# Performance work log

Hardware: AMD Instinct MI355X
Metric: run time of the kernel (lower is better)

The kernel has to match this reference:

```python
import jax, jax.numpy as jnp
import numpy as np
import math

N_HEAD = 16


def setup_inputs() -> dict:
    key = jax.random.key(0)
    ks = jax.random.split(key, 4)
    B, S, D = 4, 2048, 1024
    x = jax.random.normal(ks[0], (B, S, D), dtype=jnp.float32)
    c_attn_w = jax.random.normal(ks[1], (D, 3 * D), dtype=jnp.float32) * 0.02
    c_attn_b = jnp.zeros((3 * D,), dtype=jnp.float32)
    c_proj_w = jax.random.normal(ks[2], (D, D), dtype=jnp.float32) * 0.02
    c_proj_b = jnp.zeros((D,), dtype=jnp.float32)
    # causal mask: True where attention is disallowed (future positions)
    mask_self_attention = jnp.triu(jnp.ones((S, S), dtype=bool), k=1)[None, None]
    return {"x": x, "c_attn_w": c_attn_w, "c_attn_b": c_attn_b,
            "c_proj_w": c_proj_w, "c_proj_b": c_proj_b,
            "mask_self_attention": mask_self_attention}


def reference(x, c_attn_w, c_attn_b, c_proj_w, c_proj_b, mask_self_attention):
    B, S, D = x.shape
    H = N_HEAD
    hd = D // H
    qkv = x @ c_attn_w + c_attn_b                      # [B,S,3D]
    q, k, v = jnp.split(qkv, 3, axis=-1)
    # split heads -> [B,H,S,hd]
    q = q.reshape(B, S, H, hd).transpose(0, 2, 1, 3)
    k = k.reshape(B, S, H, hd).transpose(0, 2, 1, 3)
    v = v.reshape(B, S, H, hd).transpose(0, 2, 1, 3)
    w = jnp.einsum('bhqd,bhkd->bhqk', q, k) / math.sqrt(hd)  # scale=True
    w = jnp.where(mask_self_attention, jnp.float32(-10000.0), w)
    w = jax.nn.softmax(w, axis=-1)
    a = jnp.einsum('bhqk,bhkd->bhqd', w, v)            # [B,H,S,hd]
    a = a.transpose(0, 2, 1, 3).reshape(B, S, D)       # merge heads
    return a @ c_proj_w + c_proj_b
```

## Files before the change

kernel.cpp:

```cpp
#include <hip/hip_runtime.h>
#include <cstdint>
#include <cstddef>

#define S_LEN 2048
#define D_MODEL 1024
#define HD 64

typedef __attribute__((ext_vector_type(8))) __bf16 bf16x8;
typedef __attribute__((ext_vector_type(8))) unsigned short u16x8;
typedef __attribute__((ext_vector_type(4))) float f32x4;
typedef __attribute__((ext_vector_type(4))) unsigned short u16x4;

static __device__ __forceinline__ unsigned short f32_bf16(float f) {
    unsigned int u = __float_as_uint(f);
    u += 0x7fffu + ((u >> 16) & 1u);
    return (unsigned short)(u >> 16);
}

static __device__ __forceinline__ unsigned short f32_bf16_rn(float f) {
    return __builtin_bit_cast(unsigned short, (__bf16)f);
}

static __device__ __forceinline__ float fast_exp2(float x) {
#if __has_builtin(__builtin_amdgcn_exp2f)
    return __builtin_amdgcn_exp2f(x);
#else
    float r; asm("v_exp_f32 %0, %1" : "=v"(r) : "v"(x)); return r;
#endif
}

static __device__ __forceinline__ void gload_lds16(const void* g, void* l) {
    __builtin_amdgcn_global_load_lds(
        (const __attribute__((address_space(1))) unsigned int*)g,
        (__attribute__((address_space(3))) unsigned int*)l,
        16, 0, 0);
}

static __device__ __forceinline__ bf16x8 frag8(const unsigned short* p) {
    return __builtin_bit_cast(bf16x8, *(const u16x8*)p);
}

__global__ void prep_k(const float* __restrict__ x, unsigned short* __restrict__ xb,
                       const float* __restrict__ caw, unsigned short* __restrict__ wqt,
                       const float* __restrict__ cpw, unsigned short* __restrict__ wpt)
{
    __shared__ float tile[32][33];
    const int blk = blockIdx.x;
    const int tid = threadIdx.x;
    if (blk < 8192) {
        int i = blk * 256 + tid;
        f32x4 v = ((const f32x4*)x)[i];
        u16x4 o;
        o[0] = f32_bf16(v[0]); o[1] = f32_bf16(v[1]);
        o[2] = f32_bf16(v[2]); o[3] = f32_bf16(v[3]);
        ((u16x4*)xb)[i] = o;
        return;
    }
    const float* in; unsigned short* out; int R, C, bx, by;
    if (blk < 11264) {
        int t = blk - 8192; in = caw; out = wqt; R = 1024; C = 3072;
        bx = t % 96; by = t / 96;
    } else {
        int t = blk - 11264; in = cpw; out = wpt; R = 1024; C = 1024;
        bx = t & 31; by = t >> 5;
    }
    int tx = tid & 31, ty = tid >> 5;
    int x0 = bx * 32, y0 = by * 32;
#pragma unroll
    for (int p = 0; p < 32; p += 8)
        tile[ty + p][tx] = in[(size_t)(y0 + ty + p) * C + x0 + tx];
    __syncthreads();
#pragma unroll
    for (int p = 0; p < 32; p += 8)
        out[(size_t)(x0 + ty + p) * R + y0 + tx] = f32_bf16(tile[tx][ty + p]);
}

__device__ __forceinline__ void gemm128_mainloop(
    const unsigned short* __restrict__ A,
    const unsigned short* __restrict__ Bt,
    unsigned short* As, unsigned short* Bs,
    int m0, int n0, int Kdim, f32x4 acc[][4])
{
    const int tid = threadIdx.x;
    const int lane = tid & 63, wave = tid >> 6;
    const int wm = wave & 1, wn = wave >> 1;
    const int quad = lane >> 4, l15 = lane & 15;
    const int srow = wave * 8 + (lane >> 3);
    const int scol = ((lane & 7) ^ (lane >> 3)) * 8;
    const unsigned short* Ag = A + (size_t)(m0 + srow) * Kdim + scol;
    const unsigned short* Bg = Bt + (size_t)(n0 + srow) * Kdim + scol;
    unsigned short* Asw = As + (wave * 8) * 64 + lane * 8;
    unsigned short* Bsw = Bs + (wave * 8) * 64 + lane * 8;
    const int mkey = l15 & 7;

    for (int k0 = 0; k0 < Kdim; k0 += 64) {
        __syncthreads();
#pragma unroll
        for (int p = 0; p < 4; ++p)
            gload_lds16(Ag + (size_t)(p * 32) * Kdim + k0, Asw + (p * 32) * 64);
#pragma unroll
        for (int p = 0; p < 4; ++p)
            gload_lds16(Bg + (size_t)(p * 32) * Kdim + k0, Bsw + (p * 32) * 64);
        __syncthreads();
#pragma unroll
        for (int kh = 0; kh < 2; ++kh) {
            bf16x8 af[4], bfv[4];
#pragma unroll
            for (int i = 0; i < 4; ++i)
                af[i] = frag8(As + (wm * 64 + i * 16 + l15) * 64 +
                              ((((kh << 2) + quad) ^ mkey) << 3));
#pragma unroll
            for (int j = 0; j < 4; ++j)
                bfv[j] = frag8(Bs + (wn * 64 + j * 16 + l15) * 64 +
                               ((((kh << 2) + quad) ^ mkey) << 3));
#pragma unroll
            for (int i = 0; i < 4; ++i)
#pragma unroll
                for (int j = 0; j < 4; ++j)
                    acc[i][j] = __builtin_amdgcn_mfma_f32_16x16x32_bf16(
                        af[i], bfv[j], acc[i][j], 0, 0, 0);
        }
    }
}

__global__ __launch_bounds__(256, 2) void gemm_qkv_k(
    const unsigned short* __restrict__ xb,
    const unsigned short* __restrict__ wt,
    const float* __restrict__ bias,
    unsigned short* __restrict__ q,
    unsigned short* __restrict__ k2,
    unsigned short* __restrict__ vt)
{
    __shared__ unsigned short Sh[128 * 132];
    unsigned short* As = Sh;
    unsigned short* Bs = Sh + 128 * 64;
    const int lin = blockIdx.x + 24 * blockIdx.y;
    const int swz = (lin & 7) * 192 + (lin >> 3);
    const int n0 = (swz % 24) * 128, m0 = (swz / 24) * 128;
    f32x4 acc[4][4] = {};
    gemm128_mainloop(xb, wt, As, Bs, m0, n0, 1024, acc);

    const int tid = threadIdx.x;
    const int lane = tid & 63, wave = tid >> 6;
    const int wm = wave & 1, wn = wave >> 1;
    const int quad = lane >> 4, l15 = lane & 15;
    const bool isq = (n0 < 1024);
    const bool isv = (n0 >= 2048);
    const int cb = n0 & 1023;

    if (!isv) {
        unsigned short* outp = isq ? q : k2;
#pragma unroll
        for (int j = 0; j < 4; ++j) {
            int ct = cb + wn * 64 + j * 16 + l15;
            int h = ct >> 6, d = ct & 63;
            float bv = bias[n0 + wn * 64 + j * 16 + l15];
#pragma unroll
            for (int i = 0; i < 4; ++i)
#pragma unroll
                for (int r = 0; r < 4; ++r) {
                    int row = m0 + wm * 64 + i * 16 + quad * 4 + r;
                    int bb = row >> 11, s = row & 2047;
                    float val = acc[i][j][r] + bv;
                    if (isq) val *= 0.1803368801111244f;
                    outp[((size_t)(bb * 16 + h) * S_LEN + s) * HD + d] = f32_bf16(val);
                }
        }
    } else {
        __syncthreads();
#pragma unroll
        for (int j = 0; j < 4; ++j) {
            float bv = bias[n0 + wn * 64 + j * 16 + l15];
            int lc = wn * 64 + j * 16 + l15;
#pragma unroll
            for (int i = 0; i < 4; ++i)
#pragma unroll
                for (int r = 0; r < 4; ++r) {
                    int lr = wm * 64 + i * 16 + quad * 4 + r;
                    Sh[lr * 132 + lc] = f32_bf16(acc[i][j][r] + bv);
                }
        }
        __syncthreads();
        const int lc = (tid & 63) + (wave & 1) * 64;
        const int sh2 = wave >> 1;
        const int bb = m0 >> 11;
        const int s0 = (m0 & 2047) + sh2 * 64;
        const int bh = bb * 16 + (cb >> 6) + (lc >> 6);
        unsigned short* vp = vt + ((size_t)bh * HD + (lc & 63)) * S_LEN + s0;
#pragma unroll
        for (int k8 = 0; k8 < 8; ++k8) {
            u16x8 w;
#pragma unroll
            for (int e = 0; e < 8; ++e)
                w[e] = Sh[(sh2 * 64 + k8 * 8 + e) * 132 + lc];
            *(u16x8*)(vp + k8 * 8) = w;
        }
    }
}

__global__ __launch_bounds__(256, 2) void gemm_proj_k(
    const unsigned short* __restrict__ am,
    const unsigned short* __restrict__ wpt,
    const float* __restrict__ bias,
    float* __restrict__ out)
{
    __shared__ unsigned short As[128 * 64], Bs[128 * 64];
    const int lin = blockIdx.x + 8 * blockIdx.y;
    const int swz = (lin & 7) * 64 + (lin >> 3);
    const int n0 = (swz % 8) * 128, m0 = (swz / 8) * 128;
    f32x4 acc[4][4] = {};
    gemm128_mainloop(am, wpt, As, Bs, m0, n0, 1024, acc);

    const int lane = threadIdx.x & 63, wave = threadIdx.x >> 6;
    const int wm = wave & 1, wn = wave >> 1;
    const int quad = lane >> 4, l15 = lane & 15;
#pragma unroll
    for (int j = 0; j < 4; ++j) {
        int col = n0 + wn * 64 + j * 16 + l15;
        float bv = bias[col];
#pragma unroll
        for (int i = 0; i < 4; ++i)
#pragma unroll
            for (int r = 0; r < 4; ++r) {
                int row = m0 + wm * 64 + i * 16 + quad * 4 + r;
                out[(size_t)row * 1024 + col] = acc[i][j][r] + bv;
            }
    }
}

#define PSTR 72
__global__ __launch_bounds__(256, 3) void flash_attn_k(
    const unsigned short* __restrict__ Q,
    const unsigned short* __restrict__ K,
    const unsigned short* __restrict__ Vt,
    unsigned short* __restrict__ Am)
{
    __shared__ unsigned short Ps[4 * 32 * PSTR];
    __shared__ unsigned short Ks[2][64 * 64];
    __shared__ unsigned short Vs[2][64 * 64];

    const int bid = blockIdx.x;
    const int xcd = bid & 7;
    const int w = bid >> 3;
    const int qt = 15 - (w >> 3);
    const int bh = xcd * 8 + (w & 7);
    const int b = bh >> 4, h = bh & 15;
    const int tid = threadIdx.x;
    const int lane = tid & 63, wave = tid >> 6;
    const int quad = lane >> 4, l15 = lane & 15;

    const size_t bh_off = (size_t)bh * S_LEN * HD;
    const unsigned short* Kg = K + bh_off;
    const unsigned short* Vtg = Vt + (size_t)bh * HD * S_LEN;

    const int lrow = (lane >> 3) & 7;
    const int scol = ((lane & 7) ^ lrow) * 8;
    const int srow = wave * 8 + lrow;
    const int ldst = (wave * 8) * 64 + lane * 8;

    const int q_base = qt * 128 + wave * 32;

    bf16x8 qa[2][2];
#pragma unroll
    for (int i = 0; i < 2; ++i)
#pragma unroll
        for (int kk = 0; kk < 2; ++kk)
            qa[i][kk] = frag8(Q + bh_off +
                (size_t)(q_base + i * 16 + l15) * HD + kk * 32 + quad * 8);

    f32x4 oacc[2][4] = {};
    f32x4 lacc[2] = {};
    u16x8 ones_u = {0x3F80, 0x3F80, 0x3F80, 0x3F80, 0x3F80, 0x3F80, 0x3F80, 0x3F80};
    bf16x8 vone = __builtin_bit_cast(bf16x8, ones_u);

    const int nst = 2 * qt + 2;
    const int nst_w = nst - ((wave < 2) ? 1 : 0);
    unsigned short* pw = Ps + wave * (32 * PSTR);
    const int pkey = (l15 >> 2) & 3;
    const int kvkey = l15 & 7;

#pragma unroll
    for (int pp = 0; pp < 2; ++pp) {
        gload_lds16(Kg + (size_t)(srow + pp * 32) * HD + scol,
                    &Ks[0][ldst + (pp * 32) * 64]);
        gload_lds16(Vtg + (size_t)(srow + pp * 32) * S_LEN + scol,
                    &Vs[0][ldst + (pp * 32) * 64]);
    }
    __syncthreads();

    int cur = 0;
    for (int st = 0; st < nst; ++st) {
        if (st + 1 < nst) {
            const int nx = cur ^ 1;
            const size_t kroff = (size_t)((st + 1) * 64);
#pragma unroll
            for (int pp = 0; pp < 2; ++pp) {
                gload_lds16(Kg + (kroff + srow + pp * 32) * HD + scol,
                            &Ks[nx][ldst + (pp * 32) * 64]);
                gload_lds16(Vtg + (size_t)(srow + pp * 32) * S_LEN + kroff + scol,
                            &Vs[nx][ldst + (pp * 32) * 64]);
            }
        }
        const unsigned short* ksc = &Ks[cur][0];
        const unsigned short* vsc = &Vs[cur][0];

        if (st < nst_w) {
            f32x4 sacc[2][4] = {};
            __builtin_amdgcn_s_setprio(1);
#pragma unroll
            for (int kk = 0; kk < 2; ++kk) {
                bf16x8 kb[4];
#pragma unroll
                for (int j = 0; j < 4; ++j)
                    kb[j] = frag8(ksc + (j * 16 + l15) * 64 +
                                  ((((kk << 2) + quad) ^ kvkey) << 3));
#pragma unroll
                for (int i = 0; i < 2; ++i)
#pragma unroll
                    for (int j = 0; j < 4; ++j)
                        sacc[i][j] = __builtin_amdgcn_mfma_f32_16x16x32_bf16(
                            qa[i][kk], kb[j], sacc[i][j], 0, 0, 0);
            }
            __builtin_amdgcn_s_setprio(0);

            if (st * 64 + 63 > q_base) {
#pragma unroll
                for (int i = 0; i < 2; ++i)
#pragma unroll
                    for (int j = 0; j < 4; ++j)
#pragma unroll
                        for (int r = 0; r < 4; ++r) {
                            int kg = st * 64 + j * 16 + l15;
                            int qg = q_base + i * 16 + quad * 4 + r;
                            if (kg > qg) sacc[i][j][r] = -__builtin_inff();
                        }
            }

#pragma unroll
            for (int i = 0; i < 2; ++i)
#pragma unroll
                for (int j = 0; j < 4; ++j) {
                    int cs = ((j ^ quad) << 4) + l15;
#pragma unroll
                    for (int r = 0; r < 4; ++r)
                        pw[(i * 16 + quad * 4 + r) * PSTR + cs] =
                            f32_bf16_rn(fast_exp2(sacc[i][j][r]));
                }

#pragma unroll
            for (int kk = 0; kk < 2; ++kk) {
                bf16x8 vb[4];
#pragma unroll
                for (int d4 = 0; d4 < 4; ++d4)
                    vb[d4] = frag8(vsc + (d4 * 16 + l15) * 64 +
                                   ((((kk << 2) + quad) ^ kvkey) << 3));
                const int coff = ((((kk << 1) + (quad >> 1)) ^ pkey) << 4) + ((quad & 1) << 3);

                bf16x8 pa[2];
#pragma unroll
                for (int i = 0; i < 2; ++i)
                    pa[i] = frag8(pw + (i * 16 + l15) * PSTR + coff);
                __builtin_amdgcn_s_setprio(1);
#pragma unroll
                for (int d4 = 0; d4 < 4; ++d4)
#pragma unroll
                    for (int i = 0; i < 2; ++i)
                        oacc[i][d4] = __builtin_amdgcn_mfma_f32_16x16x32_bf16(
                            pa[i], vb[d4], oacc[i][d4], 0, 0, 0);
#pragma unroll
                for (int i = 0; i < 2; ++i)
                    lacc[i] = __builtin_amdgcn_mfma_f32_16x16x32_bf16(
                        pa[i], vone, lacc[i], 0, 0, 0);
                __builtin_amdgcn_s_setprio(0);
            }
        }

        __syncthreads();
        cur ^= 1;
    }

    unsigned short* Amp = Am + ((size_t)(b * S_LEN + q_base)) * D_MODEL + h * 64;
#pragma unroll
    for (int i = 0; i < 2; ++i)
#pragma unroll
        for (int r = 0; r < 4; ++r) {
            float inv = 1.f / lacc[i][r];
            int qloc = i * 16 + quad * 4 + r;
#pragma unroll
            for (int d4 = 0; d4 < 4; ++d4)
                Amp[(size_t)qloc * D_MODEL + d4 * 16 + l15] =
                    f32_bf16_rn(oacc[i][d4][r] * inv);
        }
}

extern "C" void kernel_launch(void* const* d_in, const int* in_sizes, int n_in,
                              void* d_out, int out_size, void* d_ws, size_t ws_size,
                              hipStream_t stream)
{
    const float* x = (const float*)d_in[0];
    const float* c_attn_w = (const float*)d_in[1];
    const float* c_attn_b = (const float*)d_in[2];
    const float* c_proj_w = (const float*)d_in[3];
    const float* c_proj_b = (const float*)d_in[4];
    float* out = (float*)d_out;

    char* ws = (char*)d_ws;
    unsigned short* xb  = (unsigned short*)(ws);
    unsigned short* q   = (unsigned short*)(ws + 16777216);
    unsigned short* k   = (unsigned short*)(ws + 33554432);
    unsigned short* vt  = (unsigned short*)(ws + 67108864);
    unsigned short* wqt = (unsigned short*)(ws + 83886080);
    unsigned short* wpt = (unsigned short*)(ws + 90177536);

    prep_k<<<12288, 256, 0, stream>>>(x, xb, c_attn_w, wqt, c_proj_w, wpt);
    gemm_qkv_k<<<dim3(24, 64), 256, 0, stream>>>(xb, wqt, c_attn_b, q, k, vt);
    flash_attn_k<<<1024, 256, 0, stream>>>(q, k, vt, xb );
    gemm_proj_k<<<dim3(8, 64), 256, 0, stream>>>(xb , wpt, c_proj_b, out);
}
```

Before: 246.2 us.

## Double-buffer LDS tiles in the shared GEMM mainloop

The GEMM mainloop now uses two LDS buffers per operand. It prefetches the next 64-wide K slice with async global-to-LDS loads while the MFMAs run on the current slice, so there is one barrier per iteration instead of two. Both the QKV and output-projection GEMMs use the new loop. The aim is to hide global load latency behind compute. In exchange, LDS per block doubles to 64KB, which may limit how many blocks fit per CU, and the loop depends on the barrier waiting for the async loads.

```diff
diff --git a/kernel.cpp b/kernel.cpp
--- a/kernel.cpp
+++ b/kernel.cpp
@@ -75,7 +75,7 @@
         out[(size_t)(x0 + ty + p) * R + y0 + tx] = f32_bf16(tile[tx][ty + p]);
 }
 
-__device__ __forceinline__ void gemm128_mainloop(
+__device__ __forceinline__ void gemm128_mainloop_db(
     const unsigned short* __restrict__ A,
     const unsigned short* __restrict__ Bt,
     unsigned short* As, unsigned short* Bs,
@@ -89,29 +89,40 @@
     const int scol = ((lane & 7) ^ (lane >> 3)) * 8;
     const unsigned short* Ag = A + (size_t)(m0 + srow) * Kdim + scol;
     const unsigned short* Bg = Bt + (size_t)(n0 + srow) * Kdim + scol;
-    unsigned short* Asw = As + (wave * 8) * 64 + lane * 8;
-    unsigned short* Bsw = Bs + (wave * 8) * 64 + lane * 8;
+    const int ldst = (wave * 8) * 64 + lane * 8;
     const int mkey = l15 & 7;
 
+#pragma unroll
+    for (int p = 0; p < 4; ++p) {
+        gload_lds16(Ag + (size_t)(p * 32) * Kdim, As + ldst + (p * 32) * 64);
+        gload_lds16(Bg + (size_t)(p * 32) * Kdim, Bs + ldst + (p * 32) * 64);
+    }
+    __syncthreads();
+
+    int cur = 0;
     for (int k0 = 0; k0 < Kdim; k0 += 64) {
-        __syncthreads();
-#pragma unroll
-        for (int p = 0; p < 4; ++p)
-            gload_lds16(Ag + (size_t)(p * 32) * Kdim + k0, Asw + (p * 32) * 64);
-#pragma unroll
-        for (int p = 0; p < 4; ++p)
-            gload_lds16(Bg + (size_t)(p * 32) * Kdim + k0, Bsw + (p * 32) * 64);
-        __syncthreads();
+        if (k0 + 64 < Kdim) {
+            const int nxo = (cur ^ 1) * 8192;
+#pragma unroll
+            for (int p = 0; p < 4; ++p) {
+                gload_lds16(Ag + (size_t)(p * 32) * Kdim + k0 + 64,
+                            As + nxo + ldst + (p * 32) * 64);
+                gload_lds16(Bg + (size_t)(p * 32) * Kdim + k0 + 64,
+                            Bs + nxo + ldst + (p * 32) * 64);
+            }
+        }
+        const unsigned short* Asc = As + cur * 8192;
+        const unsigned short* Bsc = Bs + cur * 8192;
 #pragma unroll
         for (int kh = 0; kh < 2; ++kh) {
             bf16x8 af[4], bfv[4];
 #pragma unroll
             for (int i = 0; i < 4; ++i)
-                af[i] = frag8(As + (wm * 64 + i * 16 + l15) * 64 +
+                af[i] = frag8(Asc + (wm * 64 + i * 16 + l15) * 64 +
                               ((((kh << 2) + quad) ^ mkey) << 3));
 #pragma unroll
             for (int j = 0; j < 4; ++j)
-                bfv[j] = frag8(Bs + (wn * 64 + j * 16 + l15) * 64 +
+                bfv[j] = frag8(Bsc + (wn * 64 + j * 16 + l15) * 64 +
                                ((((kh << 2) + quad) ^ mkey) << 3));
 #pragma unroll
             for (int i = 0; i < 4; ++i)
@@ -120,6 +131,8 @@
                     acc[i][j] = __builtin_amdgcn_mfma_f32_16x16x32_bf16(
                         af[i], bfv[j], acc[i][j], 0, 0, 0);
         }
+        __syncthreads();
+        cur ^= 1;
     }
 }
 
@@ -131,14 +144,14 @@
     unsigned short* __restrict__ k2,
     unsigned short* __restrict__ vt)
 {
-    __shared__ unsigned short Sh[128 * 132];
+    __shared__ unsigned short Sh[4 * 8192];
     unsigned short* As = Sh;
-    unsigned short* Bs = Sh + 128 * 64;
+    unsigned short* Bs = Sh + 2 * 8192;
     const int lin = blockIdx.x + 24 * blockIdx.y;
     const int swz = (lin & 7) * 192 + (lin >> 3);
     const int n0 = (swz % 24) * 128, m0 = (swz / 24) * 128;
     f32x4 acc[4][4] = {};
-    gemm128_mainloop(xb, wt, As, Bs, m0, n0, 1024, acc);
+    gemm128_mainloop_db(xb, wt, As, Bs, m0, n0, 1024, acc);
 
     const int tid = threadIdx.x;
     const int lane = tid & 63, wave = tid >> 6;
@@ -204,12 +217,12 @@
     const float* __restrict__ bias,
     float* __restrict__ out)
 {
-    __shared__ unsigned short As[128 * 64], Bs[128 * 64];
+    __shared__ unsigned short As[2 * 8192], Bs[2 * 8192];
     const int lin = blockIdx.x + 8 * blockIdx.y;
     const int swz = (lin & 7) * 64 + (lin >> 3);
     const int n0 = (swz % 8) * 128, m0 = (swz / 8) * 128;
     f32x4 acc[4][4] = {};
-    gemm128_mainloop(am, wpt, As, Bs, m0, n0, 1024, acc);
+    gemm128_mainloop_db(am, wpt, As, Bs, m0, n0, 1024, acc);
 
     const int lane = threadIdx.x & 63, wave = threadIdx.x >> 6;
     const int wm = wave & 1, wn = wave >> 1;
```

Result: slower. 252.6 us (+2.6%).
